# Performance work log

Measured on AMD Instinct MI355X. Metric: run time of the kernel, lower is better.

Reference implementation:

```python
import jax, jax.numpy as jnp
import numpy as np

N_HARMONICS = 100
SAMPLE_RATE = 44100
HOP_SIZE = 64
TWO_PI = 2.0 * np.pi


def setup_inputs() -> dict:
    key = jax.random.key(0)
    k1, k2, k3, k4 = jax.random.split(key, 4)
    B, T, H = 16, 500, N_HARMONICS
    f0 = jax.random.uniform(k1, (B, T, 1), dtype=jnp.float32)
    loudness = jax.random.uniform(k2, (B, T, 1), dtype=jnp.float32)
    harm_amps = jax.random.uniform(k3, (B, T, H), dtype=jnp.float32)
    harm_stretch = jax.random.uniform(k4, (B, T, 1), dtype=jnp.float32)
    return {"f0": f0, "loudness": loudness, "harm_amps": harm_amps,
            "harm_stretch": harm_stretch}


def reference(f0, loudness, harm_amps, harm_stretch):
    # harmonic indices 1..H (buffer in the torch module)
    h = jnp.arange(1, N_HARMONICS + 1, dtype=f0.dtype)  # [H]
    # prepare_harmonics
    harm = h ** (1.0 + harm_stretch)        # [B, T, H]
    harm = harm * f0                        # instantaneous harmonic freqs (Hz)
    nyquist = SAMPLE_RATE // 2
    amps = jnp.where(harm > nyquist, 0.0, harm_amps)  # in-place mask in torch
    w = harm * (TWO_PI / SAMPLE_RATE)       # radians per sample
    w = jnp.repeat(w, HOP_SIZE, axis=1)     # [B, T*hop, H]
    # generate_phases
    phases = jnp.cumsum(w, axis=1) % TWO_PI  # [B, T*hop, H]
    # generate_signal
    l = jnp.repeat(loudness, HOP_SIZE, axis=1)   # [B, T*hop, 1]
    a = jnp.repeat(amps, HOP_SIZE, axis=1)       # [B, T*hop, H]
    signal = jnp.sum(l * a * jnp.sin(phases), axis=2) / N_HARMONICS
    return signal  # [B, T*hop]
```

## Files before the change

kernel.cpp:

```cpp
#include <hip/hip_runtime.h>
#include <math.h>


#define OB_B 16
#define OB_T 500
#define OB_H 100
#define OB_HOP 64

constexpr double TWO_PI_D  = 6.283185307179586476925286766559;
constexpr double INV_2PI_D = 0.15915494309189533576888376337251;
constexpr double SR_D      = 44100.0;
constexpr float  PI_F      = 3.14159265358979f;

__global__ void __launch_bounds__(256)
ob_scan_fused(const float* __restrict__ f0,
              const float* __restrict__ stretch,
              float* __restrict__ w_f,
              float* __restrict__ base_f)
{
    int wave = threadIdx.x >> 6;
    int lane = threadIdx.x & 63;
    int bh   = blockIdx.x * 4 + wave;
    int b = bh / OB_H, h = bh % OB_H;
    double L = log2((double)(h + 1));
    const float* f0b = f0      + b * OB_T;
    const float* stb = stretch + b * OB_T;

    double w[8];
    double csum = 0.0;
    int t0 = lane * 8;
    #pragma unroll
    for (int k = 0; k < 8; ++k) {
        int t = t0 + k;
        double wv = 0.0;
        if (t < OB_T) {
            double harm = exp2((1.0 + (double)stb[t]) * L) * (double)f0b[t];
            wv = harm * (TWO_PI_D / SR_D);
        }
        w[k] = wv;
        csum += wv;
    }
    double incl = csum;
    #pragma unroll
    for (int off = 1; off < 64; off <<= 1) {
        double up = __shfl_up(incl, (unsigned)off, 64);
        if (lane >= off) incl += up;
    }
    double S = incl - csum;
    size_t rowbase = (size_t)b * OB_T * OB_H + h;
    #pragma unroll
    for (int k = 0; k < 8; ++k) {
        int t = t0 + k;
        if (t < OB_T) {
            double ph = 64.0 * S;
            ph -= TWO_PI_D * trunc(ph * INV_2PI_D);
            size_t idx = rowbase + (size_t)t * OB_H;
            base_f[idx] = (float)ph;
            w_f[idx]    = (float)w[k];
            S += w[k];
        }
    }
}

__global__ void __launch_bounds__(64)
ob_synth(const float* __restrict__ w_f,
         const float* __restrict__ base_f,
         const float* __restrict__ amps,
         const float* __restrict__ loud,
         float* __restrict__ out)
{
    int bt = blockIdx.x;
    int j  = threadIdx.x;
    __shared__ float sw[OB_H], sb[OB_H], sc[OB_H];
    size_t row = (size_t)bt * OB_H;
    float ld = loud[bt];
    for (int i = j; i < OB_H; i += 64) {
        float wv = w_f[row + i];
        sw[i] = wv;
        sb[i] = base_f[row + i];
        sc[i] = (wv > PI_F) ? 0.0f : ld * amps[row + i] * (1.0f / OB_H);
    }
    __syncthreads();
    float jf = (float)(j + 1);
    float s = 0.0f;
    #pragma unroll
    for (int h = 0; h < OB_H; ++h)
        s += sc[h] * __sinf(sb[h] + jf * sw[h]);
    out[(size_t)bt * OB_HOP + j] = s;
}

extern "C" void kernel_launch(void* const* d_in, const int* in_sizes, int n_in,
                              void* d_out, int out_size, void* d_ws, size_t ws_size,
                              hipStream_t stream)
{
    const float* f0      = (const float*)d_in[0];
    const float* loud    = (const float*)d_in[1];
    const float* amps    = (const float*)d_in[2];
    const float* stretch = (const float*)d_in[3];

    float* w_f    = (float*)d_ws;
    float* base_f = w_f + (size_t)OB_B * OB_T * OB_H;
    float* out    = (float*)d_out;

    ob_scan_fused<<<(OB_B * OB_H) / 4, 256, 0, stream>>>(f0, stretch, w_f, base_f);
    ob_synth<<<OB_B * OB_T, 64, 0, stream>>>(w_f, base_f, amps, loud, out);
}
```

Measured before the change: 84.10 us.

## Use turns-based phases, interleaved float2 buffer, and wave-level readlane synthesis

Phase and frequency are now kept in turns (cycles) instead of radians, so the hardware sin instruction (which takes turns) can be called directly and the modulo becomes a simple fractional part. Frequency and base phase go into one interleaved float2 workspace, halving the number of scattered stores and loads. The synth kernel packs four (b,t) rows per 256-thread block, one per wave. Each wave broadcasts per-harmonic coefficients with readlane instead of staging them in shared memory and syncing. The trade-off is more scalar readlane instructions in the unrolled loop, and the code relies on sinf's turns convention.

```diff
diff --git a/kernel.cpp b/kernel.cpp
--- a/kernel.cpp
+++ b/kernel.cpp
@@ -7,16 +7,16 @@
 #define OB_H 100
 #define OB_HOP 64
 
-constexpr double TWO_PI_D  = 6.283185307179586476925286766559;
-constexpr double INV_2PI_D = 0.15915494309189533576888376337251;
-constexpr double SR_D      = 44100.0;
-constexpr float  PI_F      = 3.14159265358979f;
+constexpr double SR_D = 44100.0;
+
+__device__ __forceinline__ float readlane_f(float v, int l) {
+    return __builtin_bit_cast(float, __builtin_amdgcn_readlane(__builtin_bit_cast(int, v), l));
+}
 
 __global__ void __launch_bounds__(256)
 ob_scan_fused(const float* __restrict__ f0,
               const float* __restrict__ stretch,
-              float* __restrict__ w_f,
-              float* __restrict__ base_f)
+              float2* __restrict__ wb)
 {
     int wave = threadIdx.x >> 6;
     int lane = threadIdx.x & 63;
@@ -33,10 +33,8 @@
     for (int k = 0; k < 8; ++k) {
         int t = t0 + k;
         double wv = 0.0;
-        if (t < OB_T) {
-            double harm = exp2((1.0 + (double)stb[t]) * L) * (double)f0b[t];
-            wv = harm * (TWO_PI_D / SR_D);
-        }
+        if (t < OB_T)
+            wv = exp2((1.0 + (double)stb[t]) * L) * (double)f0b[t] * (1.0 / SR_D);
         w[k] = wv;
         csum += wv;
     }
@@ -47,46 +45,57 @@
         if (lane >= off) incl += up;
     }
     double S = incl - csum;
-    size_t rowbase = (size_t)b * OB_T * OB_H + h;
     #pragma unroll
     for (int k = 0; k < 8; ++k) {
         int t = t0 + k;
         if (t < OB_T) {
             double ph = 64.0 * S;
-            ph -= TWO_PI_D * trunc(ph * INV_2PI_D);
-            size_t idx = rowbase + (size_t)t * OB_H;
-            base_f[idx] = (float)ph;
-            w_f[idx]    = (float)w[k];
+            ph -= trunc(ph);
+            wb[(size_t)(b * OB_T + t) * OB_H + h] = make_float2((float)w[k], (float)ph);
             S += w[k];
         }
     }
 }
 
-__global__ void __launch_bounds__(64)
-ob_synth(const float* __restrict__ w_f,
-         const float* __restrict__ base_f,
+__global__ void __launch_bounds__(256)
+ob_synth(const float2* __restrict__ wb,
          const float* __restrict__ amps,
          const float* __restrict__ loud,
          float* __restrict__ out)
 {
-    int bt = blockIdx.x;
-    int j  = threadIdx.x;
-    __shared__ float sw[OB_H], sb[OB_H], sc[OB_H];
-    size_t row = (size_t)bt * OB_H;
-    float ld = loud[bt];
-    for (int i = j; i < OB_H; i += 64) {
-        float wv = w_f[row + i];
-        sw[i] = wv;
-        sb[i] = base_f[row + i];
-        sc[i] = (wv > PI_F) ? 0.0f : ld * amps[row + i] * (1.0f / OB_H);
+    int wave = threadIdx.x >> 6;
+    int lane = threadIdx.x & 63;
+    int bt   = blockIdx.x * 4 + wave;
+    const float2* row  = wb   + (size_t)bt * OB_H;
+    const float*  arow = amps + (size_t)bt * OB_H;
+    float ld = loud[bt] * (1.0f / OB_H);
+
+    float2 wb0 = row[lane];
+    float  c0  = (wb0.x > 0.5f) ? 0.0f : ld * arow[lane];
+    float2 wb1 = make_float2(0.0f, 0.0f);
+    float  c1  = 0.0f;
+    if (lane < OB_H - 64) {
+        wb1 = row[64 + lane];
+        c1  = (wb1.x > 0.5f) ? 0.0f : ld * arow[64 + lane];
     }
-    __syncthreads();
-    float jf = (float)(j + 1);
-    float s = 0.0f;
+
+    float jf  = (float)(lane + 1);
+    float acc = 0.0f;
     #pragma unroll
-    for (int h = 0; h < OB_H; ++h)
-        s += sc[h] * __sinf(sb[h] + jf * sw[h]);
-    out[(size_t)bt * OB_HOP + j] = s;
+    for (int h = 0; h < 64; ++h) {
+        float w = readlane_f(wb0.x, h);
+        float b = readlane_f(wb0.y, h);
+        float c = readlane_f(c0,   h);
+        acc += c * __builtin_amdgcn_sinf(b + jf * w);
+    }
+    #pragma unroll
+    for (int h = 0; h < OB_H - 64; ++h) {
+        float w = readlane_f(wb1.x, h);
+        float b = readlane_f(wb1.y, h);
+        float c = readlane_f(c1,   h);
+        acc += c * __builtin_amdgcn_sinf(b + jf * w);
+    }
+    out[(size_t)bt * OB_HOP + lane] = acc;
 }
 
 extern "C" void kernel_launch(void* const* d_in, const int* in_sizes, int n_in,
@@ -98,10 +107,9 @@
     const float* amps    = (const float*)d_in[2];
     const float* stretch = (const float*)d_in[3];
 
-    float* w_f    = (float*)d_ws;
-    float* base_f = w_f + (size_t)OB_B * OB_T * OB_H;
-    float* out    = (float*)d_out;
+    float2* wbuf = (float2*)d_ws;
+    float*  out  = (float*)d_out;
 
-    ob_scan_fused<<<(OB_B * OB_H) / 4, 256, 0, stream>>>(f0, stretch, w_f, base_f);
-    ob_synth<<<OB_B * OB_T, 64, 0, stream>>>(w_f, base_f, amps, loud, out);
+    ob_scan_fused<<<(OB_B * OB_H) / 4, 256, 0, stream>>>(f0, stretch, wbuf);
+    ob_synth<<<(OB_B * OB_T) / 4, 256, 0, stream>>>(wbuf, amps, loud, out);
 }
```

New measurement: 87.10 us. 1.04x slower.
